# Optimization experiments

Measured on AMD Instinct MI355X. Metric: run time of the kernel, lower is better.

## Reference

```python
import jax, jax.numpy as jnp
import numpy as np

SIZE = 128   # feature dim
N = 4096     # number of mesh nodes


def setup_inputs() -> dict:
    key = jax.random.key(0)
    k_f, k_adj, k_q, k_k = jax.random.split(key, 4)
    # f: [size, N] node features (features-first, as in the torch module); scaled
    # so QK dot products stay O(1) and exp() is numerically safe.
    f = jax.random.normal(k_f, (SIZE, N), dtype=jnp.float32) * 0.1
    # neighbors: [N, N] binary adjacency with self-loops (every row sums > 0).
    adj = (jax.random.uniform(k_adj, (N, N)) < 0.005).astype(jnp.float32)
    neighbors = jnp.maximum(adj, jnp.eye(N, dtype=jnp.float32))
    # learned per-feature scale vectors (nn.init.normal_)
    wq = jax.random.normal(k_q, (SIZE,), dtype=jnp.float32)
    wk = jax.random.normal(k_k, (SIZE,), dtype=jnp.float32)
    return {"f": f, "neighbors": neighbors, "wq": wq, "wk": wk}


def reference(f, neighbors, wq, wk):
    # elementwise-scaled queries/keys: [size, N]
    wq_f = wq[:, None] * f
    wk_f = wk[:, None] * f
    # S[i, j] = exp(<wq_f[:, i], wk_f[:, j]>)  -> [N, N]
    S = jnp.exp(jnp.einsum('dn,dm->nm', wq_f, wk_f))
    # normalize by neighbor-sums: S / (neighbors @ S).T
    S = S / jnp.matmul(neighbors, S).T
    return S
```

## Files before the change

### kernel.cpp

```cpp
#include <hip/hip_runtime.h>
#include <hip/hip_fp16.h>

#define N    4096
#define SIZE 128
#define CAP  128
#define RB   16
#define TB   1024

typedef __attribute__((ext_vector_type(8))) _Float16 f16x8;
typedef __attribute__((ext_vector_type(2))) __fp16 fp16x2;
typedef __attribute__((ext_vector_type(4))) float f32x4;

__device__ __forceinline__ unsigned int pk2(float lo, float hi) {
    union { fp16x2 v; unsigned int u; } c;
    c.v = __builtin_amdgcn_cvt_pkrtz(lo, hi);
    return c.u;
}
__device__ __forceinline__ __half2 u2h(unsigned int u) {
    union { unsigned int u; __half2 h; } c; c.u = u; return c.h;
}

__global__ __launch_bounds__(256)
void build_csr(const float* __restrict__ nb, int* __restrict__ cnt4,
               int* __restrict__ idx) {
    __shared__ int sc;
    const int j    = blockIdx.x;
    const int lane = threadIdx.x & 63;
    if (threadIdx.x == 0) sc = 0;
    __syncthreads();
    const float4* row4 = (const float4*)(nb + (size_t)j * N);
    int* irow = idx + (size_t)j * CAP;

    float4 v[4];
#pragma unroll
    for (int it = 0; it < 4; ++it) v[it] = row4[threadIdx.x + it * 256];

#pragma unroll
    for (int it = 0; it < 4; ++it) {
        const float e[4] = {v[it].x, v[it].y, v[it].z, v[it].w};
#pragma unroll
        for (int q = 0; q < 4; ++q) {
            const bool nz = (e[q] != 0.0f);
            const unsigned long long m = __ballot(nz);
            if (m != 0ull) {
                int base = 0;
                if (lane == 0) base = atomicAdd(&sc, __popcll(m));
                base = __shfl(base, 0);
                if (nz) {
                    const int p = base + __popcll(m & ((1ull << lane) - 1ull));
                    const int c = 4 * (threadIdx.x + it * 256) + q;
                    if (p < CAP) irow[p] = c;
                }
            }
        }
    }
    __syncthreads();
    if (threadIdx.x == 0) {
        int n  = (sc < CAP) ? sc : CAP;
        int n4 = (n + 3) & ~3;
        for (int p = n; p < n4; ++p) irow[p] = N;
        cnt4[j] = n4 >> 2;
    }
}

__global__ __launch_bounds__(256)
void prep(const float* __restrict__ f, const float* __restrict__ wq,
          const float* __restrict__ wk, _Float16* __restrict__ Af,
          _Float16* __restrict__ Bf) {
    __shared__ float sf[SIZE][16];
    __shared__ float sqw[SIZE];
    const int t    = threadIdx.x;
    const int tile = blockIdx.x;
    if (t < SIZE) sqw[t] = wq[t] * wk[t];
    const int col0 = t & 15;
#pragma unroll
    for (int it = 0; it < 8; ++it) {
        const int k = (t >> 4) + it * 16;
        sf[k][col0] = f[(size_t)k * N + tile * 16 + col0];
    }
    __syncthreads();

    const int ks   = t >> 6;
    const int lane = t & 63;
    const int quad = lane >> 4;
    const int col  = lane & 15;
    f16x8 va, vb;
#pragma unroll
    for (int jj = 0; jj < 8; ++jj) {
        const int k = ks * 32 + quad * 8 + jj;
        const float v = sf[k][col];
        va[jj] = (_Float16)(sqw[k] * v);
        vb[jj] = (_Float16)v;
    }
    const size_t o = (size_t)(tile * 4 + ks) * 64 + lane;
    ((f16x8*)Af)[o] = va;
    ((f16x8*)Bf)[o] = vb;
}

__global__ __launch_bounds__(TB, 4)
void fused(const _Float16* __restrict__ Af, const _Float16* __restrict__ Bf,
           const int* __restrict__ cnt4, const int* __restrict__ idx,
           float* __restrict__ out) {
    __shared__ uint4 Sb[2 * N + 3];
    uint4* const sA = Sb;
    uint4* const sB = Sb + N + 2;
    const int t    = threadIdx.x;
    const int lane = t & 63;
    const int wv   = t >> 6;
    const int quad = lane >> 4;
    const int i0   = blockIdx.x * RB;

    f16x8 af[4];
    const f16x8* Ap = (const f16x8*)Af + (size_t)blockIdx.x * 4 * 64;
#pragma unroll
    for (int ks = 0; ks < 4; ++ks) af[ks] = Ap[ks * 64 + lane];
    const f16x8* Bp = (const f16x8*)Bf;

#pragma unroll 4
    for (int ti = 0; ti < 16; ++ti) {
        const int nt = wv * 16 + ti;
        f32x4 acc = {0.f, 0.f, 0.f, 0.f};
#pragma unroll
        for (int ks = 0; ks < 4; ++ks) {
            const f16x8 bfrag = Bp[(size_t)(nt * 4 + ks) * 64 + lane];
            acc = __builtin_amdgcn_mfma_f32_16x16x32_f16(af[ks], bfrag, acc, 0, 0, 0);
        }
        const int j = nt * 16 + (lane & 15);
        uint2 p;
        p.x = pk2(__expf(acc[0]), __expf(acc[1]));
        p.y = pk2(__expf(acc[2]), __expf(acc[3]));
        uint2* base = (quad < 2) ? (uint2*)&sA[j] : (uint2*)&sB[j];
        base[quad & 1] = p;
    }
    if (t == 0) {
        sA[N] = make_uint4(0u, 0u, 0u, 0u);
        sB[N] = make_uint4(0u, 0u, 0u, 0u);
    }
    __syncthreads();

    for (int u = 0; u < N / TB; ++u) {
        const int j  = t + u * TB;
        const int c4 = cnt4[j];
        const int4* irow = (const int4*)(idx + (size_t)j * CAP);
        __half2 d0[8], d1[8];
        const __half2 z = u2h(0u);
#pragma unroll
        for (int r = 0; r < 8; ++r) { d0[r] = z; d1[r] = z; }

        int4 k = irow[0];
        for (int c = 0; c < c4; ++c) {
            const int4 kn = (c + 1 < c4) ? irow[c + 1] : k;
            const uint4 ax = sA[k.x], bx = sB[k.x];
            const uint4 ay = sA[k.y], by = sB[k.y];
            const uint4 az = sA[k.z], bz = sB[k.z];
            const uint4 aw = sA[k.w], bw = sB[k.w];
            d0[0] = __hadd2(d0[0], u2h(ax.x)); d1[0] = __hadd2(d1[0], u2h(ay.x));
            d0[1] = __hadd2(d0[1], u2h(ax.y)); d1[1] = __hadd2(d1[1], u2h(ay.y));
            d0[2] = __hadd2(d0[2], u2h(ax.z)); d1[2] = __hadd2(d1[2], u2h(ay.z));
            d0[3] = __hadd2(d0[3], u2h(ax.w)); d1[3] = __hadd2(d1[3], u2h(ay.w));
            d0[4] = __hadd2(d0[4], u2h(bx.x)); d1[4] = __hadd2(d1[4], u2h(by.x));
            d0[5] = __hadd2(d0[5], u2h(bx.y)); d1[5] = __hadd2(d1[5], u2h(by.y));
            d0[6] = __hadd2(d0[6], u2h(bx.z)); d1[6] = __hadd2(d1[6], u2h(by.z));
            d0[7] = __hadd2(d0[7], u2h(bx.w)); d1[7] = __hadd2(d1[7], u2h(by.w));
            d0[0] = __hadd2(d0[0], u2h(az.x)); d1[0] = __hadd2(d1[0], u2h(aw.x));
            d0[1] = __hadd2(d0[1], u2h(az.y)); d1[1] = __hadd2(d1[1], u2h(aw.y));
            d0[2] = __hadd2(d0[2], u2h(az.z)); d1[2] = __hadd2(d1[2], u2h(aw.z));
            d0[3] = __hadd2(d0[3], u2h(az.w)); d1[3] = __hadd2(d1[3], u2h(aw.w));
            d0[4] = __hadd2(d0[4], u2h(bz.x)); d1[4] = __hadd2(d1[4], u2h(bw.x));
            d0[5] = __hadd2(d0[5], u2h(bz.y)); d1[5] = __hadd2(d1[5], u2h(bw.y));
            d0[6] = __hadd2(d0[6], u2h(bz.z)); d1[6] = __hadd2(d1[6], u2h(bw.z));
            d0[7] = __hadd2(d0[7], u2h(bz.w)); d1[7] = __hadd2(d1[7], u2h(bw.w));
            k = kn;
        }
        const uint4 na = sA[j], nb = sB[j];
        const unsigned int nu[8] = {na.x, na.y, na.z, na.w, nb.x, nb.y, nb.z, nb.w};
#pragma unroll
        for (int i = 0; i < 8; ++i) {
            const __half2 dd = __hadd2(d0[i], d1[i]);
            const __half2 nn = u2h(nu[i]);
            out[(size_t)(i0 + 2 * i + 0) * N + j] =
                __low2float(nn)  * __builtin_amdgcn_rcpf(__low2float(dd));
            out[(size_t)(i0 + 2 * i + 1) * N + j] =
                __high2float(nn) * __builtin_amdgcn_rcpf(__high2float(dd));
        }
    }
}

extern "C" void kernel_launch(void* const* d_in, const int* in_sizes, int n_in,
                              void* d_out, int out_size, void* d_ws, size_t ws_size,
                              hipStream_t stream) {
    const float* f  = (const float*)d_in[0];
    const float* nb = (const float*)d_in[1];
    const float* wq = (const float*)d_in[2];
    const float* wk = (const float*)d_in[3];
    float* out = (float*)d_out;

    int*      cnt4 = (int*)d_ws;
    int*      idx  = cnt4 + N;
    _Float16* Af   = (_Float16*)(idx + (size_t)N * CAP);
    _Float16* Bf   = Af + (size_t)256 * 4 * 64 * 8;

    build_csr<<<N, 256, 0, stream>>>(nb, cnt4, idx);
    prep<<<256, 256, 0, stream>>>(f, wq, wk, Af, Bf);
    fused<<<N / RB, TB, 0, stream>>>(Af, Bf, cnt4, idx, out);
}
```

Baseline: 167.5 us.

## Merge CSR build and prep kernels, use scan-based compaction, unroll gather by eight

Merges the CSR construction and the feature prep into one launch, so one kernel launch and its gap disappear. Replaces the per-element ballot plus shared atomic compaction with per-thread bitmasks and a wave prefix scan, so each row's indices come out in order without atomics. In the fused kernel, the neighbor gather handles eight indices per step with four accumulator sets, and the index rows for the next column are prefetched before the MFMA phase. The cost is more padding (multiples of eight), higher register pressure, and extra sentinel gathers.

Measured after the change: 145.8 us. 1.15x faster.

```diff
diff --git a/kernel.cpp b/kernel.cpp
--- a/kernel.cpp
+++ b/kernel.cpp
@@ -21,85 +21,94 @@
 }
 
 __global__ __launch_bounds__(256)
-void build_csr(const float* __restrict__ nb, int* __restrict__ cnt4,
-               int* __restrict__ idx) {
-    __shared__ int sc;
-    const int j    = blockIdx.x;
-    const int lane = threadIdx.x & 63;
-    if (threadIdx.x == 0) sc = 0;
-    __syncthreads();
-    const float4* row4 = (const float4*)(nb + (size_t)j * N);
-    int* irow = idx + (size_t)j * CAP;
-
-    float4 v[4];
-#pragma unroll
-    for (int it = 0; it < 4; ++it) v[it] = row4[threadIdx.x + it * 256];
-
-#pragma unroll
-    for (int it = 0; it < 4; ++it) {
-        const float e[4] = {v[it].x, v[it].y, v[it].z, v[it].w};
-#pragma unroll
-        for (int q = 0; q < 4; ++q) {
-            const bool nz = (e[q] != 0.0f);
-            const unsigned long long m = __ballot(nz);
-            if (m != 0ull) {
-                int base = 0;
-                if (lane == 0) base = atomicAdd(&sc, __popcll(m));
-                base = __shfl(base, 0);
-                if (nz) {
-                    const int p = base + __popcll(m & ((1ull << lane) - 1ull));
-                    const int c = 4 * (threadIdx.x + it * 256) + q;
-                    if (p < CAP) irow[p] = c;
-                }
-            }
-        }
-    }
-    __syncthreads();
-    if (threadIdx.x == 0) {
-        int n  = (sc < CAP) ? sc : CAP;
-        int n4 = (n + 3) & ~3;
-        for (int p = n; p < n4; ++p) irow[p] = N;
-        cnt4[j] = n4 >> 2;
-    }
-}
-
-__global__ __launch_bounds__(256)
-void prep(const float* __restrict__ f, const float* __restrict__ wq,
-          const float* __restrict__ wk, _Float16* __restrict__ Af,
-          _Float16* __restrict__ Bf) {
+void setup(const float* __restrict__ nb, const float* __restrict__ f,
+           const float* __restrict__ wq, const float* __restrict__ wk,
+           int* __restrict__ cnt8, int* __restrict__ idx,
+           _Float16* __restrict__ Af, _Float16* __restrict__ Bf) {
+    __shared__ int   wtot[4];
     __shared__ float sf[SIZE][16];
     __shared__ float sqw[SIZE];
-    const int t    = threadIdx.x;
-    const int tile = blockIdx.x;
-    if (t < SIZE) sqw[t] = wq[t] * wk[t];
-    const int col0 = t & 15;
-#pragma unroll
-    for (int it = 0; it < 8; ++it) {
-        const int k = (t >> 4) + it * 16;
-        sf[k][col0] = f[(size_t)k * N + tile * 16 + col0];
-    }
-    __syncthreads();
-
-    const int ks   = t >> 6;
-    const int lane = t & 63;
-    const int quad = lane >> 4;
-    const int col  = lane & 15;
-    f16x8 va, vb;
-#pragma unroll
-    for (int jj = 0; jj < 8; ++jj) {
-        const int k = ks * 32 + quad * 8 + jj;
-        const float v = sf[k][col];
-        va[jj] = (_Float16)(sqw[k] * v);
-        vb[jj] = (_Float16)v;
-    }
-    const size_t o = (size_t)(tile * 4 + ks) * 64 + lane;
-    ((f16x8*)Af)[o] = va;
-    ((f16x8*)Bf)[o] = vb;
+    const int t = threadIdx.x;
+
+    if (blockIdx.x < N) {
+        const int j    = blockIdx.x;
+        const int lane = t & 63;
+        const int wv   = t >> 6;
+        const float4* row4 = (const float4*)(nb + (size_t)j * N);
+        int* irow = idx + (size_t)j * CAP;
+
+        float4 v[4];
+#pragma unroll
+        for (int it = 0; it < 4; ++it) v[it] = row4[t + it * 256];
+
+        unsigned int msk = 0u;
+#pragma unroll
+        for (int it = 0; it < 4; ++it) {
+            const float e[4] = {v[it].x, v[it].y, v[it].z, v[it].w};
+#pragma unroll
+            for (int q = 0; q < 4; ++q)
+                if (e[q] != 0.0f) msk |= 1u << (it * 4 + q);
+        }
+        const int cnt = __popc(msk);
+        int scan = cnt;
+#pragma unroll
+        for (int s = 1; s < 64; s <<= 1) {
+            const int o = __shfl_up(scan, s);
+            if (lane >= s) scan += o;
+        }
+        if (lane == 63) wtot[wv] = scan;
+        __syncthreads();
+        int base = 0;
+#pragma unroll
+        for (int w = 0; w < 3; ++w)
+            if (w < wv) base += wtot[w];
+        int p = base + scan - cnt;
+        unsigned int m = msk;
+        while (m) {
+            const int b = __ffs(m) - 1;
+            m &= m - 1u;
+            const int c = 4 * (t + (b >> 2) * 256) + (b & 3);
+            if (p < CAP) irow[p] = c;
+            ++p;
+        }
+        if (t == 255) {
+            int n = base + scan;
+            if (n > CAP) n = CAP;
+            const int n8 = (n + 7) & ~7;
+            for (int q = n; q < n8; ++q) irow[q] = N;
+            cnt8[j] = n8 >> 3;
+        }
+    } else {
+        const int tile = blockIdx.x - N;
+        if (t < SIZE) sqw[t] = wq[t] * wk[t];
+        const int col0 = t & 15;
+#pragma unroll
+        for (int it = 0; it < 8; ++it) {
+            const int k = (t >> 4) + it * 16;
+            sf[k][col0] = f[(size_t)k * N + tile * 16 + col0];
+        }
+        __syncthreads();
+        const int ks   = t >> 6;
+        const int lane = t & 63;
+        const int quad = lane >> 4;
+        const int col  = lane & 15;
+        f16x8 va, vb;
+#pragma unroll
+        for (int jj = 0; jj < 8; ++jj) {
+            const int k = ks * 32 + quad * 8 + jj;
+            const float v = sf[k][col];
+            va[jj] = (_Float16)(sqw[k] * v);
+            vb[jj] = (_Float16)v;
+        }
+        const size_t o = (size_t)(tile * 4 + ks) * 64 + lane;
+        ((f16x8*)Af)[o] = va;
+        ((f16x8*)Bf)[o] = vb;
+    }
 }
 
 __global__ __launch_bounds__(TB, 4)
 void fused(const _Float16* __restrict__ Af, const _Float16* __restrict__ Bf,
-           const int* __restrict__ cnt4, const int* __restrict__ idx,
+           const int* __restrict__ cnt8, const int* __restrict__ idx,
            float* __restrict__ out) {
     __shared__ uint4 Sb[2 * N + 3];
     uint4* const sA = Sb;
@@ -110,6 +119,16 @@
     const int quad = lane >> 4;
     const int i0   = blockIdx.x * RB;
 
+    if (t == 0) {
+        sA[N] = make_uint4(0u, 0u, 0u, 0u);
+        sB[N] = make_uint4(0u, 0u, 0u, 0u);
+    }
+
+    int cc = cnt8[t];
+    const int4* ir0 = (const int4*)(idx + (size_t)t * CAP);
+    int4 ka = ir0[0];
+    int4 kb = ir0[1];
+
     f16x8 af[4];
     const f16x8* Ap = (const f16x8*)Af + (size_t)blockIdx.x * 4 * 64;
 #pragma unroll
@@ -126,64 +145,72 @@
             acc = __builtin_amdgcn_mfma_f32_16x16x32_f16(af[ks], bfrag, acc, 0, 0, 0);
         }
         const int j = nt * 16 + (lane & 15);
-        uint2 p;
-        p.x = pk2(__expf(acc[0]), __expf(acc[1]));
-        p.y = pk2(__expf(acc[2]), __expf(acc[3]));
-        uint2* base = (quad < 2) ? (uint2*)&sA[j] : (uint2*)&sB[j];
-        base[quad & 1] = p;
-    }
-    if (t == 0) {
-        sA[N] = make_uint4(0u, 0u, 0u, 0u);
-        sB[N] = make_uint4(0u, 0u, 0u, 0u);
+        uint2 pp;
+        pp.x = pk2(__expf(acc[0]), __expf(acc[1]));
+        pp.y = pk2(__expf(acc[2]), __expf(acc[3]));
+        uint2* bs = (quad < 2) ? (uint2*)&sA[j] : (uint2*)&sB[j];
+        bs[quad & 1] = pp;
     }
     __syncthreads();
 
-    for (int u = 0; u < N / TB; ++u) {
-        const int j  = t + u * TB;
-        const int c4 = cnt4[j];
-        const int4* irow = (const int4*)(idx + (size_t)j * CAP);
-        __half2 d0[8], d1[8];
+#define ACC(D, A, B) \
+    D[0] = __hadd2(D[0], u2h((A).x)); D[1] = __hadd2(D[1], u2h((A).y)); \
+    D[2] = __hadd2(D[2], u2h((A).z)); D[3] = __hadd2(D[3], u2h((A).w)); \
+    D[4] = __hadd2(D[4], u2h((B).x)); D[5] = __hadd2(D[5], u2h((B).y)); \
+    D[6] = __hadd2(D[6], u2h((B).z)); D[7] = __hadd2(D[7], u2h((B).w));
+
+    for (int u = 0; u < 4; ++u) {
+        const int j = t + u * TB;
+        const int4* ir = (const int4*)(idx + (size_t)j * CAP);
+        int ncc = 0; int4 nk0 = ka, nk1 = kb;
+        if (u < 3) {
+            const int jn = j + TB;
+            const int4* irn = (const int4*)(idx + (size_t)jn * CAP);
+            ncc = cnt8[jn];
+            nk0 = irn[0];
+            nk1 = irn[1];
+        }
+        __half2 d0[8], d1[8], d2[8], d3[8];
         const __half2 z = u2h(0u);
 #pragma unroll
-        for (int r = 0; r < 8; ++r) { d0[r] = z; d1[r] = z; }
-
-        int4 k = irow[0];
-        for (int c = 0; c < c4; ++c) {
-            const int4 kn = (c + 1 < c4) ? irow[c + 1] : k;
-            const uint4 ax = sA[k.x], bx = sB[k.x];
-            const uint4 ay = sA[k.y], by = sB[k.y];
-            const uint4 az = sA[k.z], bz = sB[k.z];
-            const uint4 aw = sA[k.w], bw = sB[k.w];
-            d0[0] = __hadd2(d0[0], u2h(ax.x)); d1[0] = __hadd2(d1[0], u2h(ay.x));
-            d0[1] = __hadd2(d0[1], u2h(ax.y)); d1[1] = __hadd2(d1[1], u2h(ay.y));
-            d0[2] = __hadd2(d0[2], u2h(ax.z)); d1[2] = __hadd2(d1[2], u2h(ay.z));
-            d0[3] = __hadd2(d0[3], u2h(ax.w)); d1[3] = __hadd2(d1[3], u2h(ay.w));
-            d0[4] = __hadd2(d0[4], u2h(bx.x)); d1[4] = __hadd2(d1[4], u2h(by.x));
-            d0[5] = __hadd2(d0[5], u2h(bx.y)); d1[5] = __hadd2(d1[5], u2h(by.y));
-            d0[6] = __hadd2(d0[6], u2h(bx.z)); d1[6] = __hadd2(d1[6], u2h(by.z));
-            d0[7] = __hadd2(d0[7], u2h(bx.w)); d1[7] = __hadd2(d1[7], u2h(by.w));
-            d0[0] = __hadd2(d0[0], u2h(az.x)); d1[0] = __hadd2(d1[0], u2h(aw.x));
-            d0[1] = __hadd2(d0[1], u2h(az.y)); d1[1] = __hadd2(d1[1], u2h(aw.y));
-            d0[2] = __hadd2(d0[2], u2h(az.z)); d1[2] = __hadd2(d1[2], u2h(aw.z));
-            d0[3] = __hadd2(d0[3], u2h(az.w)); d1[3] = __hadd2(d1[3], u2h(aw.w));
-            d0[4] = __hadd2(d0[4], u2h(bz.x)); d1[4] = __hadd2(d1[4], u2h(bw.x));
-            d0[5] = __hadd2(d0[5], u2h(bz.y)); d1[5] = __hadd2(d1[5], u2h(bw.y));
-            d0[6] = __hadd2(d0[6], u2h(bz.z)); d1[6] = __hadd2(d1[6], u2h(bw.z));
-            d0[7] = __hadd2(d0[7], u2h(bz.w)); d1[7] = __hadd2(d1[7], u2h(bw.w));
-            k = kn;
-        }
-        const uint4 na = sA[j], nb = sB[j];
-        const unsigned int nu[8] = {na.x, na.y, na.z, na.w, nb.x, nb.y, nb.z, nb.w};
+        for (int r = 0; r < 8; ++r) { d0[r] = z; d1[r] = z; d2[r] = z; d3[r] = z; }
+
+        for (int c = 0; c < cc; ++c) {
+            int4 pa = ka, pb = kb;
+            if (c + 1 < cc) { pa = ir[2 * c + 2]; pb = ir[2 * c + 3]; }
+            const uint4 ax = sA[ka.x], bx = sB[ka.x];
+            const uint4 ay = sA[ka.y], by = sB[ka.y];
+            const uint4 az = sA[ka.z], bz = sB[ka.z];
+            const uint4 aw = sA[ka.w], bw = sB[ka.w];
+            const uint4 ex = sA[kb.x], fx = sB[kb.x];
+            const uint4 ey = sA[kb.y], fy = sB[kb.y];
+            const uint4 ez = sA[kb.z], fz = sB[kb.z];
+            const uint4 ew = sA[kb.w], fw = sB[kb.w];
+            ACC(d0, ax, bx)
+            ACC(d1, ay, by)
+            ACC(d0, az, bz)
+            ACC(d1, aw, bw)
+            ACC(d2, ex, fx)
+            ACC(d3, ey, fy)
+            ACC(d2, ez, fz)
+            ACC(d3, ew, fw)
+            ka = pa; kb = pb;
+        }
+        const uint4 na4 = sA[j], nb4 = sB[j];
+        const unsigned int nu[8] = {na4.x, na4.y, na4.z, na4.w,
+                                    nb4.x, nb4.y, nb4.z, nb4.w};
 #pragma unroll
         for (int i = 0; i < 8; ++i) {
-            const __half2 dd = __hadd2(d0[i], d1[i]);
+            const __half2 dd = __hadd2(__hadd2(d0[i], d1[i]), __hadd2(d2[i], d3[i]));
             const __half2 nn = u2h(nu[i]);
             out[(size_t)(i0 + 2 * i + 0) * N + j] =
                 __low2float(nn)  * __builtin_amdgcn_rcpf(__low2float(dd));
             out[(size_t)(i0 + 2 * i + 1) * N + j] =
                 __high2float(nn) * __builtin_amdgcn_rcpf(__high2float(dd));
         }
-    }
+        cc = ncc; ka = nk0; kb = nk1;
+    }
+#undef ACC
 }
 
 extern "C" void kernel_launch(void* const* d_in, const int* in_sizes, int n_in,
@@ -195,12 +222,11 @@
     const float* wk = (const float*)d_in[3];
     float* out = (float*)d_out;
 
-    int*      cnt4 = (int*)d_ws;
-    int*      idx  = cnt4 + N;
+    int*      cnt8 = (int*)d_ws;
+    int*      idx  = cnt8 + N;
     _Float16* Af   = (_Float16*)(idx + (size_t)N * CAP);
     _Float16* Bf   = Af + (size_t)256 * 4 * 64 * 8;
 
-    build_csr<<<N, 256, 0, stream>>>(nb, cnt4, idx);
-    prep<<<256, 256, 0, stream>>>(f, wq, wk, Af, Bf);
-    fused<<<N / RB, TB, 0, stream>>>(Af, Bf, cnt4, idx, out);
-}
+    setup<<<N + 256, 256, 0, stream>>>(nb, f, wq, wk, cnt8, idx, Af, Bf);
+    fused<<<N / RB, TB, 0, stream>>>(Af, Bf, cnt8, idx, out);
+}
```
